# Performance work log

Hardware: AMD Instinct MI355X
Metric: run time of the kernel (lower is better)

Reference implementation:

```python
import jax, jax.numpy as jnp
import numpy as np

D_MODEL = 2048
NUM_HEADS = 16
D_KV = D_MODEL // NUM_HEADS
THETA = 10000.0


def apply_rope(x, pos):
    # x: [B, H, S, d_kv], pos: [S] int
    d = x.shape[-1]
    inv_freq = 1.0 / (THETA ** (jnp.arange(0, d, 2, dtype=jnp.float32) / d))  # [d/2]
    ang = pos.astype(jnp.float32)[:, None] * inv_freq[None, :]  # [S, d/2]
    cos, sin = jnp.cos(ang), jnp.sin(ang)  # broadcast over B,H
    x1 = x[..., 0::2]
    x2 = x[..., 1::2]
    r1 = x1 * cos - x2 * sin
    r2 = x1 * sin + x2 * cos
    return jnp.stack([r1, r2], axis=-1).reshape(x.shape)


def setup_inputs() -> dict:
    key = jax.random.key(0)
    k = jax.random.split(key, 5)
    B, S = 2, 2048
    x = jax.random.normal(k[0], (B, S, D_MODEL), dtype=jnp.float32)
    scale = 1.0 / np.sqrt(D_MODEL)
    Wq = jax.random.normal(k[1], (D_MODEL, D_MODEL), dtype=jnp.float32) * scale
    Wk = jax.random.normal(k[2], (D_MODEL, D_MODEL), dtype=jnp.float32) * scale
    Wv = jax.random.normal(k[3], (D_MODEL, D_MODEL), dtype=jnp.float32) * scale
    Wo = jax.random.normal(k[4], (D_MODEL, D_MODEL), dtype=jnp.float32) * scale
    token_position = jnp.arange(S, dtype=jnp.int64 if jax.config.jax_enable_x64 else jnp.int32)
    return {"x": x, "Wq": Wq, "Wk": Wk, "Wv": Wv, "Wo": Wo, "token_position": token_position}


def reference(x, Wq, Wk, Wv, Wo, token_position):
    B, S, _ = x.shape
    def heads(y):
        return y.reshape(B, S, NUM_HEADS, D_KV).transpose(0, 2, 1, 3)  # [B,H,S,d]
    Q = heads(jnp.einsum('bsd,df->bsf', x, Wq))
    K = heads(jnp.einsum('bsd,df->bsf', x, Wk))
    V = heads(jnp.einsum('bsd,df->bsf', x, Wv))
    Q = apply_rope(Q, token_position)
    K = apply_rope(K, token_position)
    scale = 1.0 / jnp.sqrt(jnp.asarray(D_KV, dtype=x.dtype))
    scores = jnp.einsum('bhqd,bhkd->bhqk', Q, K) * scale  # [B,H,S,S]
    causal = jnp.tril(jnp.ones((S, S), dtype=bool))
    scores = jnp.where(causal, scores, -jnp.inf)
    attn = jax.nn.softmax(scores, axis=-1)
    out = jnp.einsum('bhqk,bhkd->bhqd', attn, V)  # [B,H,S,d]
    out = out.transpose(0, 2, 1, 3).reshape(B, S, D_MODEL)
    return jnp.einsum('bsd,df->bsf', out, Wo)
```

## Files before the change

### kernel.cpp

```cpp
#include <hip/hip_runtime.h>

#define S 2048
#define DM 2048
#define NH 16
#define DH 128

typedef __attribute__((ext_vector_type(8))) short short8;
typedef __attribute__((ext_vector_type(4))) float floatx4;
typedef unsigned short u16;
typedef unsigned int u32;

__device__ __forceinline__ u16 f2bf(float f) {
  union { float f; u32 u; } v; v.f = f;
  u32 r = v.u + 0x7fffu + ((v.u >> 16) & 1u);
  return (u16)(r >> 16);
}
__device__ __forceinline__ u32 pack2(float lo, float hi) {
  return (u32)f2bf(lo) | ((u32)f2bf(hi) << 16);
}

__device__ __forceinline__ floatx4 mfma16(short8 a, short8 b, floatx4 c) {
  return __builtin_amdgcn_mfma_f32_16x16x32_bf16(a, b, c, 0, 0, 0);
}

__device__ __forceinline__ void async_cp16(const u16* g, u16* l) {
  __builtin_amdgcn_global_load_lds(
      (const __attribute__((address_space(1))) void*)g,
      (__attribute__((address_space(3))) void*)l, 16, 0, 0);
}

__global__ void conv_x_k(const float* __restrict__ x, u16* __restrict__ xb) {
  int gid = blockIdx.x * 256 + threadIdx.x;
  float4 v = ((const float4*)x)[gid];
  union { u16 u[4]; uint2 p; } o;
  o.u[0] = f2bf(v.x); o.u[1] = f2bf(v.y); o.u[2] = f2bf(v.z); o.u[3] = f2bf(v.w);
  ((uint2*)xb)[gid] = o.p;
}

__global__ void conv_w_k(const float* __restrict__ W0, const float* __restrict__ W1,
                         const float* __restrict__ W2, const float* __restrict__ W3,
                         u16* __restrict__ out) {
  __shared__ float tile[32][33];
  const float* W = blockIdx.z == 0 ? W0 : blockIdx.z == 1 ? W1 : blockIdx.z == 2 ? W2 : W3;
  u16* O = out + (size_t)blockIdx.z * DM * DM;
  int tx = threadIdx.x & 31, ty = threadIdx.x >> 5;
  int k0 = blockIdx.y * 32, n0 = blockIdx.x * 32;
#pragma unroll
  for (int j = 0; j < 4; j++)
    tile[ty + j * 8][tx] = W[(size_t)(k0 + ty + j * 8) * DM + n0 + tx];
  __syncthreads();
#pragma unroll
  for (int j = 0; j < 4; j++)
    O[(size_t)(n0 + ty + j * 8) * DM + k0 + tx] = f2bf(tile[tx][ty + j * 8]);
}

__global__ __launch_bounds__(256, 4)
void gemm_k(const u16* __restrict__ A, const u16* __restrict__ Wt,
            u16* __restrict__ oQ, u16* __restrict__ oK, u16* __restrict__ oV,
            float* __restrict__ oO, const int* __restrict__ tp, int opmode)
{
  __shared__ u16 As[128 * 32];
  __shared__ u16 Bs[128 * 32];
  const int t = threadIdx.x;
  const int w = t >> 6, lane = t & 63;
  const int l16 = lane & 15, quad = lane >> 4;
  const int m0 = blockIdx.y * 128, n0 = blockIdx.x * 128;
  const int wm = (w >> 1) * 64, wn = (w & 1) * 64;
  const u16* Bt = Wt + (size_t)(opmode == 1 ? 3 : blockIdx.z) * DM * DM;

  const u16* pA[2]; const u16* pB[2]; u16* lA[2]; u16* lB[2];
#pragma unroll
  for (int i = 0; i < 2; i++) {
    int unit = i * 256 + t;
    int row = unit >> 2, s = unit & 3;
    int c = s ^ ((row >> 1) & 3);
    pA[i] = A + (size_t)(m0 + row) * DM + c * 8;
    pB[i] = Bt + (size_t)(n0 + row) * DM + c * 8;
    lA[i] = &As[unit * 8];
    lB[i] = &Bs[unit * 8];
  }

  floatx4 acc[4][4] = {};

  for (int k0 = 0; k0 < DM; k0 += 32) {
#pragma unroll
    for (int i = 0; i < 2; i++) {
      async_cp16(pA[i] + k0, lA[i]);
      async_cp16(pB[i] + k0, lB[i]);
    }
    __syncthreads();
    short8 af[4], bfr[4];
#pragma unroll
    for (int i = 0; i < 4; i++) {
      int row = wm + i * 16 + l16;
      af[i] = *(short8*)&As[(row * 4 + (quad ^ ((row >> 1) & 3))) * 8];
    }
#pragma unroll
    for (int i = 0; i < 4; i++) {
      int row = wn + i * 16 + l16;
      bfr[i] = *(short8*)&Bs[(row * 4 + (quad ^ ((row >> 1) & 3))) * 8];
    }
#pragma unroll
    for (int mi = 0; mi < 4; mi++)
#pragma unroll
      for (int ni = 0; ni < 4; ni++)
        acc[mi][ni] = mfma16(af[mi], bfr[ni], acc[mi][ni]);
    __syncthreads();
  }

  const int mode = (opmode == 1) ? 3 : ((int)blockIdx.z == 2 ? 2 : 0);
  if (mode == 3) {
#pragma unroll
    for (int mi = 0; mi < 4; mi++) {
      int m = m0 + wm + mi * 16 + quad * 4;
#pragma unroll
      for (int ni = 0; ni < 4; ni++) {
        int n = n0 + wn + ni * 16 + l16;
#pragma unroll
        for (int r = 0; r < 4; r++)
          oO[(size_t)(m + r) * DM + n] = acc[mi][ni][r];
      }
    }
  } else if (mode == 2) {
#pragma unroll
    for (int mi = 0; mi < 4; mi++) {
      int m = m0 + wm + mi * 16 + quad * 4;
      int b = m >> 11, s = m & (S - 1);
#pragma unroll
      for (int ni = 0; ni < 4; ni++) {
        int f = n0 + wn + ni * 16 + l16;
        int h = f >> 7, dh = f & (DH - 1);
        union { u16 u[4]; uint2 p; } pk;
#pragma unroll
        for (int r = 0; r < 4; r++) pk.u[r] = f2bf(acc[mi][ni][r]);
        *(uint2*)&oV[((size_t)(b * NH + h) * DH + dh) * S + s] = pk.p;
      }
    }
  } else {
    u16* Out = ((int)blockIdx.z == 0) ? oQ : oK;
    const float qs = ((int)blockIdx.z == 0) ? 0.12752780f : 1.0f;
#pragma unroll
    for (int mi = 0; mi < 4; mi++) {
#pragma unroll
      for (int r = 0; r < 4; r++) {
        int m = m0 + wm + mi * 16 + quad * 4 + r;
        int b = m >> 11, s = m & (S - 1);
        int ps = tp[s];
#pragma unroll
        for (int ni = 0; ni < 4; ni++) {
          int f = n0 + wn + ni * 16 + l16;
          int h = f >> 7, dh = f & (DH - 1);
          float own = acc[mi][ni][r];
          float oth = __shfl_xor(own, 1, 64);
          float fr = __expf((float)(dh & ~1) * (-9.210340371976184f / 128.0f));
          float ang = (float)ps * fr;
          float sn, cs; __sincosf(ang, &sn, &cs);
          float res = (dh & 1) ? (oth * sn + own * cs) : (own * cs - oth * sn);
          Out[((size_t)(b * NH + h) * S + s) * DH + dh] = f2bf(res * qs);
        }
      }
    }
  }
}

__global__ __launch_bounds__(256, 2)
void attn_k(const u16* __restrict__ Q, const u16* __restrict__ K,
            const u16* __restrict__ Vt, u16* __restrict__ O)
{
  __shared__ u16 Ks[64 * 128];
  __shared__ u16 Vs[128 * 64];
  __shared__ u16 P[4][32 * 72];
  const int t = threadIdx.x, w = t >> 6, lane = t & 63;
  const int l16 = lane & 15, quad = lane >> 4;
  const int task = blockIdx.x;
  const int bh = task & 31, b = bh >> 4, h = bh & 15;
  const int g = 15 - (task >> 5);
  const int qg = g * 128;
  const int qt = qg + w * 32;
  const u16* Qb = Q + (size_t)bh * S * DH;
  const u16* Kb = K + (size_t)bh * S * DH;
  const u16* Vb = Vt + (size_t)bh * DH * S;
  u16* Pw = P[w];

  const u16* pK[4]; u16* lK[4];
  const u16* pV[4]; u16* lV[4];
#pragma unroll
  for (int j = 0; j < 4; j++) {
    int kr = w * 16 + j * 4 + (lane >> 4);
    int ks = lane & 15;
    int kc = ks ^ (kr & 15);
    pK[j] = Kb + (size_t)kr * DH + kc * 8;
    lK[j] = &Ks[kr * 128 + ks * 8];
    int vr = w * 32 + j * 8 + (lane >> 3);
    int vs = lane & 7;
    int vc = vs ^ (vr & 7);
    pV[j] = Vb + (size_t)vr * S + vc * 8;
    lV[j] = &Vs[vr * 64 + vs * 8];
  }

  short8 aq0[4], aq1[4];
#pragma unroll
  for (int kc = 0; kc < 4; kc++) {
    aq0[kc] = *(const short8*)&Qb[(size_t)(qt + l16) * DH + kc * 32 + quad * 8];
    aq1[kc] = *(const short8*)&Qb[(size_t)(qt + 16 + l16) * DH + kc * 32 + quad * 8];
  }

  floatx4 o0[8] = {}, o1[8] = {};
  float m0_ = -3.0e38f, l0_ = 0.0f, m1_ = -3.0e38f, l1_ = 0.0f;
  const int kend = qg + 128;

  for (int k0 = 0; k0 < kend; k0 += 64) {
#pragma unroll
    for (int j = 0; j < 4; j++) async_cp16(pK[j] + (size_t)k0 * DH, lK[j]);
#pragma unroll
    for (int j = 0; j < 4; j++) async_cp16(pV[j] + k0, lV[j]);
    __syncthreads();

    if (k0 < qt + 32) {
      floatx4 s0[4] = {}, s1[4] = {};
#pragma unroll
      for (int hh = 0; hh < 4; hh++) {
        int row = hh * 16 + l16;
#pragma unroll
        for (int kc = 0; kc < 4; kc++) {
          short8 kf = *(short8*)&Ks[row * 128 + (((kc * 4 + quad) ^ l16) << 3)];
          s0[hh] = mfma16(kf, aq0[kc], s0[hh]);
          s1[hh] = mfma16(kf, aq1[kc], s1[hh]);
        }
      }
      if (k0 + 64 > qt) {
#pragma unroll
        for (int hh = 0; hh < 4; hh++)
#pragma unroll
          for (int r = 0; r < 4; r++) {
            int j = k0 + hh * 16 + quad * 4 + r;
            if (j > qt + l16) s0[hh][r] = -3.0e38f;
            if (j > qt + 16 + l16) s1[hh][r] = -3.0e38f;
          }
      }
      {
        float mloc = -3.0e38f;
#pragma unroll
        for (int hh = 0; hh < 4; hh++)
          mloc = fmaxf(mloc, fmaxf(fmaxf(s0[hh][0], s0[hh][1]), fmaxf(s0[hh][2], s0[hh][3])));
        mloc = fmaxf(mloc, __shfl_xor(mloc, 16, 64));
        mloc = fmaxf(mloc, __shfl_xor(mloc, 32, 64));
        float nm = fmaxf(m0_, mloc);
        float al = __builtin_amdgcn_exp2f(m0_ - nm);
        m0_ = nm;
        float sl = 0.0f;
#pragma unroll
        for (int hh = 0; hh < 4; hh++) {
          float e0 = __builtin_amdgcn_exp2f(s0[hh][0] - nm);
          float e1 = __builtin_amdgcn_exp2f(s0[hh][1] - nm);
          float e2 = __builtin_amdgcn_exp2f(s0[hh][2] - nm);
          float e3 = __builtin_amdgcn_exp2f(s0[hh][3] - nm);
          sl += (e0 + e1) + (e2 + e3);
          uint2 pk; pk.x = pack2(e0, e1); pk.y = pack2(e2, e3);
          *(uint2*)&Pw[l16 * 72 + hh * 16 + quad * 4] = pk;
        }
        float ts = sl + __shfl_xor(sl, 16, 64);
        ts += __shfl_xor(ts, 32, 64);
        l0_ = l0_ * al + ts;
#pragma unroll
        for (int t8 = 0; t8 < 8; t8++)
#pragma unroll
          for (int r = 0; r < 4; r++) o0[t8][r] *= al;
      }
      {
        float mloc = -3.0e38f;
#pragma unroll
        for (int hh = 0; hh < 4; hh++)
          mloc = fmaxf(mloc, fmaxf(fmaxf(s1[hh][0], s1[hh][1]), fmaxf(s1[hh][2], s1[hh][3])));
        mloc = fmaxf(mloc, __shfl_xor(mloc, 16, 64));
        mloc = fmaxf(mloc, __shfl_xor(mloc, 32, 64));
        float nm = fmaxf(m1_, mloc);
        float al = __builtin_amdgcn_exp2f(m1_ - nm);
        m1_ = nm;
        float sl = 0.0f;
#pragma unroll
        for (int hh = 0; hh < 4; hh++) {
          float e0 = __builtin_amdgcn_exp2f(s1[hh][0] - nm);
          float e1 = __builtin_amdgcn_exp2f(s1[hh][1] - nm);
          float e2 = __builtin_amdgcn_exp2f(s1[hh][2] - nm);
          float e3 = __builtin_amdgcn_exp2f(s1[hh][3] - nm);
          sl += (e0 + e1) + (e2 + e3);
          uint2 pk; pk.x = pack2(e0, e1); pk.y = pack2(e2, e3);
          *(uint2*)&Pw[(16 + l16) * 72 + hh * 16 + quad * 4] = pk;
        }
        float ts = sl + __shfl_xor(sl, 16, 64);
        ts += __shfl_xor(ts, 32, 64);
        l1_ = l1_ * al + ts;
#pragma unroll
        for (int t8 = 0; t8 < 8; t8++)
#pragma unroll
          for (int r = 0; r < 4; r++) o1[t8][r] *= al;
      }
      asm volatile("s_waitcnt lgkmcnt(0)" ::: "memory");
#pragma unroll
      for (int c = 0; c < 2; c++) {
        short8 pf0 = *(short8*)&Pw[l16 * 72 + c * 32 + quad * 8];
        short8 pf1 = *(short8*)&Pw[(16 + l16) * 72 + c * 32 + quad * 8];
#pragma unroll
        for (int t8 = 0; t8 < 8; t8++) {
          int row = t8 * 16 + l16;
          short8 av = *(short8*)&Vs[row * 64 + (((c * 4 + quad) ^ (l16 & 7)) << 3)];
          o0[t8] = mfma16(av, pf0, o0[t8]);
          o1[t8] = mfma16(av, pf1, o1[t8]);
        }
      }
    }
    __syncthreads();
  }

  float inv0 = __builtin_amdgcn_rcpf(l0_);
  float inv1 = __builtin_amdgcn_rcpf(l1_);
#pragma unroll
  for (int t8 = 0; t8 < 8; t8++) {
    union { u16 u[4]; uint2 p; } pa, pb;
#pragma unroll
    for (int r = 0; r < 4; r++) {
      pa.u[r] = f2bf(o0[t8][r] * inv0);
      pb.u[r] = f2bf(o1[t8][r] * inv1);
    }
    *(uint2*)&O[((size_t)(b * S + qt + l16)) * DM + h * DH + t8 * 16 + quad * 4] = pa.p;
    *(uint2*)&O[((size_t)(b * S + qt + 16 + l16)) * DM + h * DH + t8 * 16 + quad * 4] = pb.p;
  }
}

extern "C" void kernel_launch(void* const* d_in, const int* in_sizes, int n_in,
                              void* d_out, int out_size, void* d_ws, size_t ws_size,
                              hipStream_t stream) {
  const float* x  = (const float*)d_in[0];
  const float* Wq = (const float*)d_in[1];
  const float* Wk = (const float*)d_in[2];
  const float* Wv = (const float*)d_in[3];
  const float* Wo = (const float*)d_in[4];
  const int*   tp = (const int*)d_in[5];

  char* ws = (char*)d_ws;
  u16* Wt = (u16*)ws;
  u16* xb = (u16*)(ws + 33554432);
  u16* Qb = (u16*)(ws + 50331648);
  u16* Kb = (u16*)(ws + 67108864);
  u16* Vb = (u16*)(ws + 83886080);
  u16* Ob = (u16*)(ws + 100663296);

  conv_x_k<<<8192, 256, 0, stream>>>(x, xb);
  conv_w_k<<<dim3(64, 64, 4), 256, 0, stream>>>(Wq, Wk, Wv, Wo, Wt);
  gemm_k<<<dim3(16, 32, 3), 256, 0, stream>>>(xb, Wt, Qb, Kb, Vb, nullptr, tp, 0);
  attn_k<<<512, 256, 0, stream>>>(Qb, Kb, Vb, Ob);
  gemm_k<<<dim3(16, 32, 1), 256, 0, stream>>>(Ob, Wt, nullptr, nullptr, nullptr,
                                              (float*)d_out, tp, 1);
}
```

Measured before the change: 387.1 us.

## Use packed bf16 conversion, skip unneeded rescales, raise attention occupancy

Replaces the manual bf16 rounding with the HIP packed float2-to-bfloat162 conversion in the conversion, V-projection, softmax P and output paths, which may map to a hardware packed-convert instruction. The online-softmax output rescale is now skipped whenever no lane in the wave saw its running max increase. The attention kernel's launch bounds go from 2 to 3 blocks per CU. The higher bound forces a tighter register budget and may cause spills, and the new wave-level branch adds a small cost to each key tile.

```diff
diff --git a/kernel.cpp b/kernel.cpp
--- a/kernel.cpp
+++ b/kernel.cpp
@@ -1,4 +1,5 @@
 #include <hip/hip_runtime.h>
+#include <hip/hip_bf16.h>
 
 #define S 2048
 #define DM 2048
@@ -16,7 +17,10 @@
   return (u16)(r >> 16);
 }
 __device__ __forceinline__ u32 pack2(float lo, float hi) {
-  return (u32)f2bf(lo) | ((u32)f2bf(hi) << 16);
+  float2 f; f.x = lo; f.y = hi;
+  __hip_bfloat162 h = __float22bfloat162_rn(f);
+  union { __hip_bfloat162 h; u32 u; } c; c.h = h;
+  return c.u;
 }
 
 __device__ __forceinline__ floatx4 mfma16(short8 a, short8 b, floatx4 c) {
@@ -32,9 +36,8 @@
 __global__ void conv_x_k(const float* __restrict__ x, u16* __restrict__ xb) {
   int gid = blockIdx.x * 256 + threadIdx.x;
   float4 v = ((const float4*)x)[gid];
-  union { u16 u[4]; uint2 p; } o;
-  o.u[0] = f2bf(v.x); o.u[1] = f2bf(v.y); o.u[2] = f2bf(v.z); o.u[3] = f2bf(v.w);
-  ((uint2*)xb)[gid] = o.p;
+  uint2 p; p.x = pack2(v.x, v.y); p.y = pack2(v.z, v.w);
+  ((uint2*)xb)[gid] = p;
 }
 
 __global__ void conv_w_k(const float* __restrict__ W0, const float* __restrict__ W1,
@@ -130,10 +133,9 @@
       for (int ni = 0; ni < 4; ni++) {
         int f = n0 + wn + ni * 16 + l16;
         int h = f >> 7, dh = f & (DH - 1);
-        union { u16 u[4]; uint2 p; } pk;
-#pragma unroll
-        for (int r = 0; r < 4; r++) pk.u[r] = f2bf(acc[mi][ni][r]);
-        *(uint2*)&oV[((size_t)(b * NH + h) * DH + dh) * S + s] = pk.p;
+        uint2 p; p.x = pack2(acc[mi][ni][0], acc[mi][ni][1]);
+        p.y = pack2(acc[mi][ni][2], acc[mi][ni][3]);
+        *(uint2*)&oV[((size_t)(b * NH + h) * DH + dh) * S + s] = p;
       }
     }
   } else {
@@ -163,7 +165,7 @@
   }
 }
 
-__global__ __launch_bounds__(256, 2)
+__global__ __launch_bounds__(256, 3)
 void attn_k(const u16* __restrict__ Q, const u16* __restrict__ K,
             const u16* __restrict__ Vt, u16* __restrict__ O)
 {
@@ -245,7 +247,8 @@
           mloc = fmaxf(mloc, fmaxf(fmaxf(s0[hh][0], s0[hh][1]), fmaxf(s0[hh][2], s0[hh][3])));
         mloc = fmaxf(mloc, __shfl_xor(mloc, 16, 64));
         mloc = fmaxf(mloc, __shfl_xor(mloc, 32, 64));
-        float nm = fmaxf(m0_, mloc);
+        bool upd = mloc > m0_;
+        float nm = upd ? mloc : m0_;
         float al = __builtin_amdgcn_exp2f(m0_ - nm);
         m0_ = nm;
         float sl = 0.0f;
@@ -262,10 +265,12 @@
         float ts = sl + __shfl_xor(sl, 16, 64);
         ts += __shfl_xor(ts, 32, 64);
         l0_ = l0_ * al + ts;
-#pragma unroll
-        for (int t8 = 0; t8 < 8; t8++)
-#pragma unroll
-          for (int r = 0; r < 4; r++) o0[t8][r] *= al;
+        if (__any(upd && k0 > 0)) {
+#pragma unroll
+          for (int t8 = 0; t8 < 8; t8++)
+#pragma unroll
+            for (int r = 0; r < 4; r++) o0[t8][r] *= al;
+        }
       }
       {
         float mloc = -3.0e38f;
@@ -274,7 +279,8 @@
           mloc = fmaxf(mloc, fmaxf(fmaxf(s1[hh][0], s1[hh][1]), fmaxf(s1[hh][2], s1[hh][3])));
         mloc = fmaxf(mloc, __shfl_xor(mloc, 16, 64));
         mloc = fmaxf(mloc, __shfl_xor(mloc, 32, 64));
-        float nm = fmaxf(m1_, mloc);
+        bool upd = mloc > m1_;
+        float nm = upd ? mloc : m1_;
         float al = __builtin_amdgcn_exp2f(m1_ - nm);
         m1_ = nm;
         float sl = 0.0f;
@@ -291,10 +297,12 @@
         float ts = sl + __shfl_xor(sl, 16, 64);
         ts += __shfl_xor(ts, 32, 64);
         l1_ = l1_ * al + ts;
-#pragma unroll
-        for (int t8 = 0; t8 < 8; t8++)
-#pragma unroll
-          for (int r = 0; r < 4; r++) o1[t8][r] *= al;
+        if (__any(upd && k0 > 0)) {
+#pragma unroll
+          for (int t8 = 0; t8 < 8; t8++)
+#pragma unroll
+            for (int r = 0; r < 4; r++) o1[t8][r] *= al;
+        }
       }
       asm volatile("s_waitcnt lgkmcnt(0)" ::: "memory");
 #pragma unroll
@@ -317,14 +325,13 @@
   float inv1 = __builtin_amdgcn_rcpf(l1_);
 #pragma unroll
   for (int t8 = 0; t8 < 8; t8++) {
-    union { u16 u[4]; uint2 p; } pa, pb;
-#pragma unroll
-    for (int r = 0; r < 4; r++) {
-      pa.u[r] = f2bf(o0[t8][r] * inv0);
-      pb.u[r] = f2bf(o1[t8][r] * inv1);
-    }
-    *(uint2*)&O[((size_t)(b * S + qt + l16)) * DM + h * DH + t8 * 16 + quad * 4] = pa.p;
-    *(uint2*)&O[((size_t)(b * S + qt + 16 + l16)) * DM + h * DH + t8 * 16 + quad * 4] = pb.p;
+    uint2 pa, pb;
+    pa.x = pack2(o0[t8][0] * inv0, o0[t8][1] * inv0);
+    pa.y = pack2(o0[t8][2] * inv0, o0[t8][3] * inv0);
+    pb.x = pack2(o1[t8][0] * inv1, o1[t8][1] * inv1);
+    pb.y = pack2(o1[t8][2] * inv1, o1[t8][3] * inv1);
+    *(uint2*)&O[((size_t)(b * S + qt + l16)) * DM + h * DH + t8 * 16 + quad * 4] = pa;
+    *(uint2*)&O[((size_t)(b * S + qt + 16 + l16)) * DM + h * DH + t8 * 16 + quad * 4] = pb;
   }
 }
 
```

After: 410.6 us. 1.06x slower.
